# Kernel tuning notes

Hardware: AMD Instinct MI355X
Metric: run time of the kernel (lower is better)

The kernel has to match this reference:

```python
import jax, jax.numpy as jnp
import numpy as np

N_NODES = 100000
N_EDGES = 1600000
IN_CH, HID_CH, OUT_CH = 128, 128, 64
N_GRAPHS = 64


def gcn_conv(x, src, dst, W, b, n_nodes):
    """PyG-style GCNConv: self-loops already included in (src, dst).
    out_i = b + sum_j norm_ij * (x_j @ W), norm_ij = deg_i^-1/2 * deg_j^-1/2."""
    xw = x @ W  # [N, out]
    deg = jax.ops.segment_sum(jnp.ones_like(dst, dtype=xw.dtype), dst,
                              num_segments=n_nodes)  # [N]
    dinv = jnp.where(deg > 0, jax.lax.rsqrt(jnp.maximum(deg, 1e-12)), 0.0)
    norm = dinv[src] * dinv[dst]  # [E]
    msg = xw[src] * norm[:, None]  # gather + scale  [E, out]
    out = jax.ops.segment_sum(msg, dst, num_segments=n_nodes)  # scatter-add
    return out + b


def global_mean_pool(x, batch, n_graphs):
    s = jax.ops.segment_sum(x, batch, num_segments=n_graphs)
    cnt = jax.ops.segment_sum(jnp.ones((x.shape[0],), x.dtype), batch,
                              num_segments=n_graphs)
    return s / jnp.maximum(cnt, 1.0)[:, None]


def setup_inputs() -> dict:
    key = jax.random.key(0)
    ks = jax.random.split(key, 9)
    x = jax.random.normal(ks[0], (N_NODES, IN_CH), dtype=jnp.float32)
    edge_index = jax.random.randint(ks[1], (2, N_EDGES), 0, N_NODES, dtype=jnp.int64)
    batch = jnp.sort(jax.random.randint(ks[2], (N_NODES,), 0, N_GRAPHS, dtype=jnp.int64))
    # Glorot-ish params
    s1 = 1.0 / np.sqrt(IN_CH)
    s2 = 1.0 / np.sqrt(HID_CH)
    W1 = jax.random.normal(ks[3], (IN_CH, HID_CH), jnp.float32) * s1
    b1 = jnp.zeros((HID_CH,), jnp.float32)
    W2 = jax.random.normal(ks[4], (HID_CH, HID_CH), jnp.float32) * s2
    b2 = jnp.zeros((HID_CH,), jnp.float32)
    Wl = jax.random.normal(ks[5], (HID_CH, OUT_CH), jnp.float32) * s2
    bl = jax.random.normal(ks[6], (OUT_CH,), jnp.float32) * 0.01
    return {"x": x, "edge_index": edge_index, "batch": batch,
            "W1": W1, "b1": b1, "W2": W2, "b2": b2, "Wl": Wl, "bl": bl}


def reference(x, edge_index, batch, W1, b1, W2, b2, Wl, bl):
    n = x.shape[0]
    loop = jnp.arange(n, dtype=edge_index.dtype)
    src = jnp.concatenate([edge_index[0], loop])  # add self-loops
    dst = jnp.concatenate([edge_index[1], loop])
    h = jax.nn.relu(gcn_conv(x, src, dst, W1, b1, n))
    h = jax.nn.relu(gcn_conv(h, src, dst, W2, b2, n))
    g = global_mean_pool(h, batch, N_GRAPHS)  # [B, hid]
    return g @ Wl + bl  # [B, out]
```

## Files before the change

kernel.cpp:

```cpp
#include <hip/hip_runtime.h>

#define N_NODESC 100000
#define N_EDGESC 1600000
#define CH 128
#define NG 64
#define OC 64

#define GST_BLKS 391
#define MFMA_BLKS 1563
#define PAD_STRIDE 64
#define SENTINEL N_NODESC

#define BIN_SHIFT 9
#define BIN_W 512
#define NBINS 196
#define BIN_CAP 16384
#define BIN1_BLKS 391
#define E_PER_BIN1 4096

typedef __attribute__((ext_vector_type(8))) short short8;
typedef __attribute__((ext_vector_type(4))) float f32x4;

__device__ __forceinline__ unsigned short f2b_u(float f) {
    union { float f; unsigned int u; } x; x.f = f;
    unsigned int u = x.u;
    return (unsigned short)((u + 0x7fffu + ((u >> 16) & 1u)) >> 16);
}
__device__ __forceinline__ float b2f_lo(unsigned int v) {
    union { unsigned int u; float f; } x; x.u = v << 16; return x.f;
}
__device__ __forceinline__ float b2f_hi(unsigned int v) {
    union { unsigned int u; float f; } x; x.u = v & 0xffff0000u; return x.f;
}

#define WSTR 136
template<int AFP>
__device__ __forceinline__ void mfma_compute(int blk, int t, const void* __restrict__ Ap,
                                             signed char* __restrict__ Oq,
                                             float* __restrict__ osc,
                                             const unsigned short* WsT) {
    int wave = t >> 6, lane = t & 63;
    int quad = lane >> 4, l16 = lane & 15;
    int arow = blk * 64 + wave * 16 + l16;
    bool rowok = arow < N_NODESC;
    f32x4 acc[8] = {};
#pragma unroll
    for (int c = 0; c < 4; ++c) {
        int koff = c * 32 + quad * 8;
        short8 a;
        if (AFP) {
            const float* A = (const float*)Ap;
            float4 f0 = make_float4(0, 0, 0, 0), f1 = make_float4(0, 0, 0, 0);
            if (rowok) {
                f0 = *(const float4*)(A + (size_t)arow * 128 + koff);
                f1 = *(const float4*)(A + (size_t)arow * 128 + koff + 4);
            }
            a[0] = (short)f2b_u(f0.x); a[1] = (short)f2b_u(f0.y);
            a[2] = (short)f2b_u(f0.z); a[3] = (short)f2b_u(f0.w);
            a[4] = (short)f2b_u(f1.x); a[5] = (short)f2b_u(f1.y);
            a[6] = (short)f2b_u(f1.z); a[7] = (short)f2b_u(f1.w);
        } else {
            const unsigned short* A = (const unsigned short*)Ap;
            if (rowok) a = *(const short8*)(A + (size_t)arow * 128 + koff);
            else       a = (short8)(short)0;
        }
#pragma unroll
        for (int tt = 0; tt < 8; ++tt) {
            short8 b = *(const short8*)&WsT[(tt * 16 + l16) * WSTR + koff];
            acc[tt] = __builtin_amdgcn_mfma_f32_16x16x32_bf16(a, b, acc[tt], 0, 0, 0);
        }
    }
    int orow0 = blk * 64 + wave * 16 + quad * 4;
#pragma unroll
    for (int r = 0; r < 4; ++r) {
        int g = orow0 + r;
        float m = 0.f;
#pragma unroll
        for (int tt = 0; tt < 8; ++tt) m = fmaxf(m, fabsf(acc[tt][r]));
        m = fmaxf(m, __shfl_xor(m, 1));
        m = fmaxf(m, __shfl_xor(m, 2));
        m = fmaxf(m, __shfl_xor(m, 4));
        m = fmaxf(m, __shfl_xor(m, 8));
        float inv = m > 0.f ? 127.f / m : 0.f;
        if (g < N_NODESC) {
#pragma unroll
            for (int tt = 0; tt < 8; ++tt)
                Oq[(size_t)g * 128 + tt * 16 + l16] = (signed char)(int)rintf(acc[tt][r] * inv);
            if (l16 == 0) osc[g] = m * (1.f / 127.f);
        }
    }
}

__global__ __launch_bounds__(256) void k_pre(const int* __restrict__ ei,
                                             const int* __restrict__ batch,
                                             const float* __restrict__ W1,
                                             const float* __restrict__ W2,
                                             int* __restrict__ cursor,
                                             unsigned int* __restrict__ binbuf,
                                             unsigned short* __restrict__ Wt1,
                                             unsigned short* __restrict__ Wt2,
                                             int* __restrict__ gstart,
                                             float* __restrict__ xsc) {
    __shared__ int hist[NBINS];
    int b = blockIdx.x, t = threadIdx.x;
    if (b < BIN1_BLKS) {
        for (int i = t; i < NBINS; i += 256) hist[i] = 0;
        __syncthreads();
        int e0 = b * E_PER_BIN1;
#pragma unroll 4
        for (int i = 0; i < E_PER_BIN1 / 256; ++i) {
            int e = e0 + i * 256 + t;
            if (e < N_EDGESC) atomicAdd(&hist[ei[N_EDGESC + e] >> BIN_SHIFT], 1);
        }
        __syncthreads();
        for (int i = t; i < NBINS; i += 256) {
            int c = hist[i];
            hist[i] = c ? atomicAdd(&cursor[i], c) : 0;
        }
        __syncthreads();
#pragma unroll 4
        for (int i = 0; i < E_PER_BIN1 / 256; ++i) {
            int e = e0 + i * 256 + t;
            if (e < N_EDGESC) {
                int d = ei[N_EDGESC + e];
                int s = ei[e];
                int bin = d >> BIN_SHIFT;
                int off = atomicAdd(&hist[bin], 1);
                binbuf[(size_t)bin * BIN_CAP + off] =
                    ((unsigned int)(d & (BIN_W - 1)) << 17) | (unsigned int)s;
            }
        }
    } else if (b < BIN1_BLKS + 64) {
        int i = (b - BIN1_BLKS) * 256 + t;
        int k = i >> 7, c = i & 127;
        Wt1[c * 128 + k] = f2b_u(W1[k * 128 + c]);
    } else if (b < BIN1_BLKS + 128) {
        int i = (b - BIN1_BLKS - 64) * 256 + t;
        int k = i >> 7, c = i & 127;
        Wt2[c * 128 + k] = f2b_u(W2[k * 128 + c]);
    } else {
        int i = (b - BIN1_BLKS - 128) * 256 + t;
        if (i >= N_NODESC) {
            if (i == N_NODESC) xsc[SENTINEL] = 0.f;
            return;
        }
        int bb = batch[i];
        int bp = (i == 0) ? -1 : batch[i - 1];
        for (int g = bp + 1; g <= bb; ++g) gstart[g] = i;
        if (i == N_NODESC - 1)
            for (int g = bb + 1; g <= NG; ++g) gstart[g] = N_NODESC;
    }
}

__global__ __launch_bounds__(256) void k_main(const float* __restrict__ x,
                                              const unsigned short* __restrict__ Wt1,
                                              signed char* __restrict__ xwq,
                                              float* __restrict__ xsc,
                                              const int* __restrict__ cursor,
                                              const unsigned int* __restrict__ binbuf,
                                              int* __restrict__ deg,
                                              float* __restrict__ dinvt,
                                              int* __restrict__ pad) {
    __shared__ unsigned short WsT[128 * WSTR];
    int t = threadIdx.x;
    if (blockIdx.x < NBINS) {
        int bin = blockIdx.x;
        if (bin == 0 && t == 0) dinvt[SENTINEL] = 0.f;
        int* ldeg = (int*)WsT;
        for (int i = t; i < BIN_W; i += 256) ldeg[i] = 0;
        __syncthreads();
        int n = cursor[bin];
        size_t base = (size_t)bin * BIN_CAP;
        for (int i = t; i < n; i += 256) {
            unsigned int rec = binbuf[base + i];
            int dl = rec >> 17;
            int s = rec & 0x1FFFF;
            int slot = atomicAdd(&ldeg[dl], 1) & (PAD_STRIDE - 1);
            pad[(size_t)((bin << BIN_SHIFT) + dl) * PAD_STRIDE + slot] = s;
        }
        __syncthreads();
        for (int i = t; i < BIN_W; i += 256) {
            int node = (bin << BIN_SHIFT) + i;
            if (node < N_NODESC) {
                int dg = ldeg[i];
                if (dg > PAD_STRIDE) dg = PAD_STRIDE;
                deg[node] = dg;
                dinvt[node] = rsqrtf((float)(dg + 1));
                int r8 = (dg + 7) & ~7;
                for (int j = dg; j < r8; ++j)
                    pad[(size_t)node * PAD_STRIDE + j] = SENTINEL;
            }
        }
    } else {
        int blk = blockIdx.x - NBINS;
        const uint4* wsrc = (const uint4*)Wt1;
        for (int idx = t; idx < 2048; idx += 256) {
            int row = idx >> 4, sub = idx & 15;
            *((uint4*)&WsT[row * WSTR] + sub) = wsrc[row * 16 + sub];
        }
        __syncthreads();
        mfma_compute<1>(blk, t, x, xwq, xsc, WsT);
    }
}

__global__ __launch_bounds__(256) void k_mfma2(const unsigned short* __restrict__ A,
                                               const unsigned short* __restrict__ Wt,
                                               signed char* __restrict__ Oq,
                                               float* __restrict__ osc) {
    __shared__ unsigned short WsT[128 * WSTR];
    int t = threadIdx.x;
    {
        const uint4* wsrc = (const uint4*)Wt;
        for (int idx = t; idx < 2048; idx += 256) {
            int row = idx >> 4, sub = idx & 15;
            *((uint4*)&WsT[row * WSTR] + sub) = wsrc[row * 16 + sub];
        }
    }
    __syncthreads();
    mfma_compute<0>(blockIdx.x, t, A, Oq, osc, WsT);
}

#define ACCQ(lo, hi, wk)                                                    \
    acc[0] += wk * (float)((int)((lo) << 24) >> 24);                        \
    acc[1] += wk * (float)((int)((lo) << 16) >> 24);                        \
    acc[2] += wk * (float)((int)((lo) <<  8) >> 24);                        \
    acc[3] += wk * (float)((int)(lo) >> 24);                                \
    acc[4] += wk * (float)((int)((hi) << 24) >> 24);                        \
    acc[5] += wk * (float)((int)((hi) << 16) >> 24);                        \
    acc[6] += wk * (float)((int)((hi) <<  8) >> 24);                        \
    acc[7] += wk * (float)((int)(hi) >> 24);

__device__ __forceinline__ void group_accum(const signed char* __restrict__ xwq,
                                            const float* __restrict__ dinvt,
                                            const float* __restrict__ xsc,
                                            const int* __restrict__ pad,
                                            int base, int l16, int n8,
                                            float* acc) {
    if (n8 <= 0) return;
    const int4* prow = (const int4*)&pad[base];
    int4 p0 = prow[0], p1 = prow[1];
    for (int kb = 0; kb < n8; ++kb) {
        int s[8] = {p0.x, p0.y, p0.z, p0.w, p1.x, p1.y, p1.z, p1.w};
        float w[8];
        uint2 v[8];
#pragma unroll
        for (int k = 0; k < 8; ++k) {
            w[k] = dinvt[s[k]] * xsc[s[k]];
            v[k] = *(const uint2*)&xwq[(size_t)(unsigned int)s[k] * 128 + l16 * 8];
        }
        int nk = (kb + 1 < n8) ? kb + 1 : kb;
        int4 q0 = prow[nk * 2], q1 = prow[nk * 2 + 1];
#pragma unroll
        for (int k = 0; k < 8; ++k) {
            ACCQ(v[k].x, v[k].y, w[k])
        }
        p0 = q0; p1 = q1;
    }
}

__global__ __launch_bounds__(256) void k_gather1(const signed char* __restrict__ xwq,
                                                 const float* __restrict__ xsc,
                                                 const int* __restrict__ deg,
                                                 const float* __restrict__ dinvt,
                                                 const int* __restrict__ pad,
                                                 const float* __restrict__ bias,
                                                 unsigned int* __restrict__ outp) {
    int t = threadIdx.x;
    int lane = t & 63, w = t >> 6;
    int g = lane >> 4, l16 = lane & 15;
    int node = blockIdx.x * 16 + w * 4 + g;
    int dg = deg[node];
    float wn = dinvt[node];
    float wsn = wn * xsc[node];
    uint2 vs = *(const uint2*)&xwq[(size_t)(unsigned int)node * 128 + l16 * 8];
    float acc[8] = {0.f, 0.f, 0.f, 0.f, 0.f, 0.f, 0.f, 0.f};
    ACCQ(vs.x, vs.y, wsn)
    group_accum(xwq, dinvt, xsc, pad, node * PAD_STRIDE, l16, (dg + 7) >> 3, acc);
    float4 bA = *(const float4*)&bias[l16 * 8];
    float4 bB = *(const float4*)&bias[l16 * 8 + 4];
    float o0 = fmaxf(bA.x + wn * acc[0], 0.f);
    float o1 = fmaxf(bA.y + wn * acc[1], 0.f);
    float o2 = fmaxf(bA.z + wn * acc[2], 0.f);
    float o3 = fmaxf(bA.w + wn * acc[3], 0.f);
    float o4 = fmaxf(bB.x + wn * acc[4], 0.f);
    float o5 = fmaxf(bB.y + wn * acc[5], 0.f);
    float o6 = fmaxf(bB.z + wn * acc[6], 0.f);
    float o7 = fmaxf(bB.w + wn * acc[7], 0.f);
    uint4 ov;
    ov.x = ((unsigned int)f2b_u(o1) << 16) | (unsigned int)f2b_u(o0);
    ov.y = ((unsigned int)f2b_u(o3) << 16) | (unsigned int)f2b_u(o2);
    ov.z = ((unsigned int)f2b_u(o5) << 16) | (unsigned int)f2b_u(o4);
    ov.w = ((unsigned int)f2b_u(o7) << 16) | (unsigned int)f2b_u(o6);
    *(uint4*)&outp[(unsigned int)node * 64 + l16 * 4] = ov;
}

__global__ __launch_bounds__(256) void k_gather_pool(const signed char* __restrict__ xwq,
                                                     const float* __restrict__ xsc,
                                                     const int* __restrict__ deg,
                                                     const float* __restrict__ dinvt,
                                                     const int* __restrict__ pad,
                                                     const float* __restrict__ bias,
                                                     const int* __restrict__ batch,
                                                     float* __restrict__ gpart) {
    __shared__ float lds[4 * 128];
    int t = threadIdx.x, w = t >> 6, lane = t & 63;
    int g = lane >> 4, l16 = lane & 15;
    int base = blockIdx.x * 16;
    int node = base + w * 4 + g;
    int dg = deg[node];
    float wn = dinvt[node];
    float wsn = wn * xsc[node];
    uint2 vs = *(const uint2*)&xwq[(size_t)(unsigned int)node * 128 + l16 * 8];
    float acc[8] = {0.f, 0.f, 0.f, 0.f, 0.f, 0.f, 0.f, 0.f};
    ACCQ(vs.x, vs.y, wsn)
    group_accum(xwq, dinvt, xsc, pad, node * PAD_STRIDE, l16, (dg + 7) >> 3, acc);
    float4 bA = *(const float4*)&bias[l16 * 8];
    float4 bB = *(const float4*)&bias[l16 * 8 + 4];
    float o[8];
    o[0] = fmaxf(bA.x + wn * acc[0], 0.f);
    o[1] = fmaxf(bA.y + wn * acc[1], 0.f);
    o[2] = fmaxf(bA.z + wn * acc[2], 0.f);
    o[3] = fmaxf(bA.w + wn * acc[3], 0.f);
    o[4] = fmaxf(bB.x + wn * acc[4], 0.f);
    o[5] = fmaxf(bB.y + wn * acc[5], 0.f);
    o[6] = fmaxf(bB.z + wn * acc[6], 0.f);
    o[7] = fmaxf(bB.w + wn * acc[7], 0.f);
    bool fast = batch[base] == batch[base + 15];
    if (fast) {
#pragma unroll
        for (int j = 0; j < 8; ++j) {
            float v = o[j];
            v += __shfl_xor(v, 16);
            v += __shfl_xor(v, 32);
            o[j] = v;
        }
        if (lane < 16) {
#pragma unroll
            for (int j = 0; j < 8; ++j) lds[w * 128 + l16 * 8 + j] = o[j];
        }
        __syncthreads();
        if (t < 128) {
            float v = lds[t] + lds[128 + t] + lds[256 + t] + lds[384 + t];
            atomicAdd(&gpart[batch[base] * 128 + t], v);
        }
    } else {
        int gb = batch[node];
#pragma unroll
        for (int j = 0; j < 8; ++j)
            atomicAdd(&gpart[gb * 128 + l16 * 8 + j], o[j]);
    }
}

__global__ void k_final(const float* __restrict__ gpart, const int* __restrict__ gstart,
                        const float* __restrict__ Wl, const float* __restrict__ bl,
                        float* __restrict__ out) {
    __shared__ float gs[128];
    int b = blockIdx.x;
    int o = threadIdx.x;
    gs[o] = gpart[b * 128 + o];
    gs[o + 64] = gpart[b * 128 + 64 + o];
    __syncthreads();
    int cnt = gstart[b + 1] - gstart[b];
    float sc = 1.f / (float)(cnt > 0 ? cnt : 1);
    float sum = 0.f;
    for (int k = 0; k < 128; ++k) sum += gs[k] * Wl[k * 64 + o];
    out[b * 64 + o] = bl[o] + sc * sum;
}

extern "C" void kernel_launch(void* const* d_in, const int* in_sizes, int n_in,
                              void* d_out, int out_size, void* d_ws, size_t ws_size,
                              hipStream_t stream) {
    const float* x    = (const float*)d_in[0];
    const int*   ei   = (const int*)d_in[1];
    const int*   batch= (const int*)d_in[2];
    const float* W1   = (const float*)d_in[3];
    const float* b1   = (const float*)d_in[4];
    const float* W2   = (const float*)d_in[5];
    const float* b2   = (const float*)d_in[6];
    const float* Wl   = (const float*)d_in[7];
    const float* bl   = (const float*)d_in[8];
    float* out = (float*)d_out;

    char* ws = (char*)d_ws;
    signed char* xwq = (signed char*)ws; ws += (size_t)(N_NODESC + 1) * CH;
    unsigned short* h_b = (unsigned short*)ws; ws += (size_t)N_NODESC * CH * 2;
    unsigned short* Wt1 = (unsigned short*)ws; ws += (size_t)CH * CH * 2;
    unsigned short* Wt2 = (unsigned short*)ws; ws += (size_t)CH * CH * 2;
    int*   cursor = (int*)ws;   ws += (size_t)NBINS * 4;
    float* gpart  = (float*)ws; ws += (size_t)NG * CH * 4;
    int*   deg    = (int*)ws;   ws += (size_t)N_NODESC * 4;
    float* dinvt  = (float*)ws; ws += (size_t)(N_NODESC + 4) * 4;
    float* xsc    = (float*)ws; ws += (size_t)(N_NODESC + 4) * 4;
    int*   pad    = (int*)ws;   ws += (size_t)N_NODESC * PAD_STRIDE * 4;
    unsigned int* binbuf = (unsigned int*)ws; ws += (size_t)NBINS * BIN_CAP * 4;
    int*   gstart = (int*)ws;   ws += (NG + 8) * 4;

    hipMemsetAsync(cursor, 0, (size_t)NBINS * 4 + (size_t)NG * CH * 4, stream);

    k_pre<<<BIN1_BLKS + 128 + GST_BLKS, 256, 0, stream>>>(ei, batch, W1, W2,
        cursor, binbuf, Wt1, Wt2, gstart, xsc);
    k_main<<<NBINS + MFMA_BLKS, 256, 0, stream>>>(x, Wt1, xwq, xsc, cursor, binbuf,
                                                  deg, dinvt, pad);

    k_gather1<<<N_NODESC / 16, 256, 0, stream>>>(xwq, xsc, deg, dinvt, pad, b1,
                                                 (unsigned int*)h_b);
    k_mfma2<<<MFMA_BLKS, 256, 0, stream>>>(h_b, Wt2, xwq, xsc);
    k_gather_pool<<<N_NODESC / 16, 256, 0, stream>>>(xwq, xsc, deg, dinvt, pad, b2,
                                                     batch, gpart);

    k_final<<<NG, 64, 0, stream>>>(gpart, gstart, Wl, bl, out);
}
```

Before: 293.4 us.

## Process two nodes per lane group and precompute per-node gather weights

Each 16-lane group in the two gather kernels now accumulates two destination nodes with interleaved neighbor batches, and the grid is halved. This is meant to put more independent loads in flight per thread and hide gather latency. A new small kernel precomputes dinv*scale per node before each gather, so every neighbor needs one weight load instead of two. The cost is two extra kernel launches, higher register pressure, and divergence when the two nodes have different degrees.

```diff
diff --git a/kernel.cpp b/kernel.cpp
--- a/kernel.cpp
+++ b/kernel.cpp
@@ -25,12 +25,6 @@
     union { float f; unsigned int u; } x; x.f = f;
     unsigned int u = x.u;
     return (unsigned short)((u + 0x7fffu + ((u >> 16) & 1u)) >> 16);
-}
-__device__ __forceinline__ float b2f_lo(unsigned int v) {
-    union { unsigned int u; float f; } x; x.u = v << 16; return x.f;
-}
-__device__ __forceinline__ float b2f_hi(unsigned int v) {
-    union { unsigned int u; float f; } x; x.u = v & 0xffff0000u; return x.f;
 }
 
 #define WSTR 136
@@ -220,46 +214,43 @@
     mfma_compute<0>(blockIdx.x, t, A, Oq, osc, WsT);
 }
 
-#define ACCQ(lo, hi, wk)                                                    \
-    acc[0] += wk * (float)((int)((lo) << 24) >> 24);                        \
-    acc[1] += wk * (float)((int)((lo) << 16) >> 24);                        \
-    acc[2] += wk * (float)((int)((lo) <<  8) >> 24);                        \
-    acc[3] += wk * (float)((int)(lo) >> 24);                                \
-    acc[4] += wk * (float)((int)((hi) << 24) >> 24);                        \
-    acc[5] += wk * (float)((int)((hi) << 16) >> 24);                        \
-    acc[6] += wk * (float)((int)((hi) <<  8) >> 24);                        \
-    acc[7] += wk * (float)((int)(hi) >> 24);
-
-__device__ __forceinline__ void group_accum(const signed char* __restrict__ xwq,
-                                            const float* __restrict__ dinvt,
-                                            const float* __restrict__ xsc,
-                                            const int* __restrict__ pad,
-                                            int base, int l16, int n8,
-                                            float* acc) {
-    if (n8 <= 0) return;
-    const int4* prow = (const int4*)&pad[base];
-    int4 p0 = prow[0], p1 = prow[1];
-    for (int kb = 0; kb < n8; ++kb) {
-        int s[8] = {p0.x, p0.y, p0.z, p0.w, p1.x, p1.y, p1.z, p1.w};
-        float w[8];
-        uint2 v[8];
-#pragma unroll
-        for (int k = 0; k < 8; ++k) {
-            w[k] = dinvt[s[k]] * xsc[s[k]];
-            v[k] = *(const uint2*)&xwq[(size_t)(unsigned int)s[k] * 128 + l16 * 8];
-        }
-        int nk = (kb + 1 < n8) ? kb + 1 : kb;
-        int4 q0 = prow[nk * 2], q1 = prow[nk * 2 + 1];
-#pragma unroll
-        for (int k = 0; k < 8; ++k) {
-            ACCQ(v[k].x, v[k].y, w[k])
-        }
-        p0 = q0; p1 = q1;
-    }
+__global__ __launch_bounds__(256) void k_wsc(const float* __restrict__ dinvt,
+                                             const float* __restrict__ xsc,
+                                             float* __restrict__ wsc) {
+    int i = blockIdx.x * 256 + threadIdx.x;
+    if (i <= N_NODESC) wsc[i] = dinvt[i] * xsc[i];
+}
+
+__device__ __forceinline__ void accq(float* acc, unsigned int lo, unsigned int hi, float wk) {
+    acc[0] += wk * (float)((int)(lo << 24) >> 24);
+    acc[1] += wk * (float)((int)(lo << 16) >> 24);
+    acc[2] += wk * (float)((int)(lo <<  8) >> 24);
+    acc[3] += wk * (float)((int)lo >> 24);
+    acc[4] += wk * (float)((int)(hi << 24) >> 24);
+    acc[5] += wk * (float)((int)(hi << 16) >> 24);
+    acc[6] += wk * (float)((int)(hi <<  8) >> 24);
+    acc[7] += wk * (float)((int)hi >> 24);
+}
+
+__device__ __forceinline__ void accum8(const signed char* __restrict__ xwq,
+                                       const float* __restrict__ wsc,
+                                       const int4* __restrict__ prow,
+                                       int kb, int l16, float* acc) {
+    int4 p0 = prow[kb * 2], p1 = prow[kb * 2 + 1];
+    int s[8] = {p0.x, p0.y, p0.z, p0.w, p1.x, p1.y, p1.z, p1.w};
+    float w[8];
+    uint2 v[8];
+#pragma unroll
+    for (int k = 0; k < 8; ++k) {
+        w[k] = wsc[s[k]];
+        v[k] = *(const uint2*)&xwq[(size_t)(unsigned int)s[k] * 128 + l16 * 8];
+    }
+#pragma unroll
+    for (int k = 0; k < 8; ++k) accq(acc, v[k].x, v[k].y, w[k]);
 }
 
 __global__ __launch_bounds__(256) void k_gather1(const signed char* __restrict__ xwq,
-                                                 const float* __restrict__ xsc,
+                                                 const float* __restrict__ wsc,
                                                  const int* __restrict__ deg,
                                                  const float* __restrict__ dinvt,
                                                  const int* __restrict__ pad,
@@ -268,34 +259,51 @@
     int t = threadIdx.x;
     int lane = t & 63, w = t >> 6;
     int g = lane >> 4, l16 = lane & 15;
-    int node = blockIdx.x * 16 + w * 4 + g;
-    int dg = deg[node];
-    float wn = dinvt[node];
-    float wsn = wn * xsc[node];
-    uint2 vs = *(const uint2*)&xwq[(size_t)(unsigned int)node * 128 + l16 * 8];
-    float acc[8] = {0.f, 0.f, 0.f, 0.f, 0.f, 0.f, 0.f, 0.f};
-    ACCQ(vs.x, vs.y, wsn)
-    group_accum(xwq, dinvt, xsc, pad, node * PAD_STRIDE, l16, (dg + 7) >> 3, acc);
+    int nA = blockIdx.x * 32 + w * 8 + g * 2;
+    int nB = nA + 1;
+    int dgA = deg[nA], dgB = deg[nB];
+    float wnA = dinvt[nA], wnB = dinvt[nB];
+    float wsA = wsc[nA], wsB = wsc[nB];
+    uint2 vsA = *(const uint2*)&xwq[(size_t)(unsigned int)nA * 128 + l16 * 8];
+    uint2 vsB = *(const uint2*)&xwq[(size_t)(unsigned int)nB * 128 + l16 * 8];
+    float accA[8] = {0.f, 0.f, 0.f, 0.f, 0.f, 0.f, 0.f, 0.f};
+    float accB[8] = {0.f, 0.f, 0.f, 0.f, 0.f, 0.f, 0.f, 0.f};
+    accq(accA, vsA.x, vsA.y, wsA);
+    accq(accB, vsB.x, vsB.y, wsB);
+    int nbA = (dgA + 7) >> 3, nbB = (dgB + 7) >> 3;
+    int nmax = nbA > nbB ? nbA : nbB;
+    const int4* prA = (const int4*)&pad[nA * PAD_STRIDE];
+    const int4* prB = (const int4*)&pad[nB * PAD_STRIDE];
+    for (int kb = 0; kb < nmax; ++kb) {
+        if (kb < nbA) accum8(xwq, wsc, prA, kb, l16, accA);
+        if (kb < nbB) accum8(xwq, wsc, prB, kb, l16, accB);
+    }
     float4 bA = *(const float4*)&bias[l16 * 8];
     float4 bB = *(const float4*)&bias[l16 * 8 + 4];
-    float o0 = fmaxf(bA.x + wn * acc[0], 0.f);
-    float o1 = fmaxf(bA.y + wn * acc[1], 0.f);
-    float o2 = fmaxf(bA.z + wn * acc[2], 0.f);
-    float o3 = fmaxf(bA.w + wn * acc[3], 0.f);
-    float o4 = fmaxf(bB.x + wn * acc[4], 0.f);
-    float o5 = fmaxf(bB.y + wn * acc[5], 0.f);
-    float o6 = fmaxf(bB.z + wn * acc[6], 0.f);
-    float o7 = fmaxf(bB.w + wn * acc[7], 0.f);
-    uint4 ov;
-    ov.x = ((unsigned int)f2b_u(o1) << 16) | (unsigned int)f2b_u(o0);
-    ov.y = ((unsigned int)f2b_u(o3) << 16) | (unsigned int)f2b_u(o2);
-    ov.z = ((unsigned int)f2b_u(o5) << 16) | (unsigned int)f2b_u(o4);
-    ov.w = ((unsigned int)f2b_u(o7) << 16) | (unsigned int)f2b_u(o6);
-    *(uint4*)&outp[(unsigned int)node * 64 + l16 * 4] = ov;
+    float oA[8], oB[8];
+    oA[0] = fmaxf(bA.x + wnA * accA[0], 0.f); oA[1] = fmaxf(bA.y + wnA * accA[1], 0.f);
+    oA[2] = fmaxf(bA.z + wnA * accA[2], 0.f); oA[3] = fmaxf(bA.w + wnA * accA[3], 0.f);
+    oA[4] = fmaxf(bB.x + wnA * accA[4], 0.f); oA[5] = fmaxf(bB.y + wnA * accA[5], 0.f);
+    oA[6] = fmaxf(bB.z + wnA * accA[6], 0.f); oA[7] = fmaxf(bB.w + wnA * accA[7], 0.f);
+    oB[0] = fmaxf(bA.x + wnB * accB[0], 0.f); oB[1] = fmaxf(bA.y + wnB * accB[1], 0.f);
+    oB[2] = fmaxf(bA.z + wnB * accB[2], 0.f); oB[3] = fmaxf(bA.w + wnB * accB[3], 0.f);
+    oB[4] = fmaxf(bB.x + wnB * accB[4], 0.f); oB[5] = fmaxf(bB.y + wnB * accB[5], 0.f);
+    oB[6] = fmaxf(bB.z + wnB * accB[6], 0.f); oB[7] = fmaxf(bB.w + wnB * accB[7], 0.f);
+    uint4 ovA, ovB;
+    ovA.x = ((unsigned int)f2b_u(oA[1]) << 16) | (unsigned int)f2b_u(oA[0]);
+    ovA.y = ((unsigned int)f2b_u(oA[3]) << 16) | (unsigned int)f2b_u(oA[2]);
+    ovA.z = ((unsigned int)f2b_u(oA[5]) << 16) | (unsigned int)f2b_u(oA[4]);
+    ovA.w = ((unsigned int)f2b_u(oA[7]) << 16) | (unsigned int)f2b_u(oA[6]);
+    ovB.x = ((unsigned int)f2b_u(oB[1]) << 16) | (unsigned int)f2b_u(oB[0]);
+    ovB.y = ((unsigned int)f2b_u(oB[3]) << 16) | (unsigned int)f2b_u(oB[2]);
+    ovB.z = ((unsigned int)f2b_u(oB[5]) << 16) | (unsigned int)f2b_u(oB[4]);
+    ovB.w = ((unsigned int)f2b_u(oB[7]) << 16) | (unsigned int)f2b_u(oB[6]);
+    *(uint4*)&outp[(unsigned int)nA * 64 + l16 * 4] = ovA;
+    *(uint4*)&outp[(unsigned int)nB * 64 + l16 * 4] = ovB;
 }
 
 __global__ __launch_bounds__(256) void k_gather_pool(const signed char* __restrict__ xwq,
-                                                     const float* __restrict__ xsc,
+                                                     const float* __restrict__ wsc,
                                                      const int* __restrict__ deg,
                                                      const float* __restrict__ dinvt,
                                                      const int* __restrict__ pad,
@@ -305,38 +313,49 @@
     __shared__ float lds[4 * 128];
     int t = threadIdx.x, w = t >> 6, lane = t & 63;
     int g = lane >> 4, l16 = lane & 15;
-    int base = blockIdx.x * 16;
-    int node = base + w * 4 + g;
-    int dg = deg[node];
-    float wn = dinvt[node];
-    float wsn = wn * xsc[node];
-    uint2 vs = *(const uint2*)&xwq[(size_t)(unsigned int)node * 128 + l16 * 8];
-    float acc[8] = {0.f, 0.f, 0.f, 0.f, 0.f, 0.f, 0.f, 0.f};
-    ACCQ(vs.x, vs.y, wsn)
-    group_accum(xwq, dinvt, xsc, pad, node * PAD_STRIDE, l16, (dg + 7) >> 3, acc);
+    int base = blockIdx.x * 32;
+    int nA = base + w * 8 + g * 2;
+    int nB = nA + 1;
+    int dgA = deg[nA], dgB = deg[nB];
+    float wnA = dinvt[nA], wnB = dinvt[nB];
+    float wsA = wsc[nA], wsB = wsc[nB];
+    uint2 vsA = *(const uint2*)&xwq[(size_t)(unsigned int)nA * 128 + l16 * 8];
+    uint2 vsB = *(const uint2*)&xwq[(size_t)(unsigned int)nB * 128 + l16 * 8];
+    float accA[8] = {0.f, 0.f, 0.f, 0.f, 0.f, 0.f, 0.f, 0.f};
+    float accB[8] = {0.f, 0.f, 0.f, 0.f, 0.f, 0.f, 0.f, 0.f};
+    accq(accA, vsA.x, vsA.y, wsA);
+    accq(accB, vsB.x, vsB.y, wsB);
+    int nbA = (dgA + 7) >> 3, nbB = (dgB + 7) >> 3;
+    int nmax = nbA > nbB ? nbA : nbB;
+    const int4* prA = (const int4*)&pad[nA * PAD_STRIDE];
+    const int4* prB = (const int4*)&pad[nB * PAD_STRIDE];
+    for (int kb = 0; kb < nmax; ++kb) {
+        if (kb < nbA) accum8(xwq, wsc, prA, kb, l16, accA);
+        if (kb < nbB) accum8(xwq, wsc, prB, kb, l16, accB);
+    }
     float4 bA = *(const float4*)&bias[l16 * 8];
     float4 bB = *(const float4*)&bias[l16 * 8 + 4];
-    float o[8];
-    o[0] = fmaxf(bA.x + wn * acc[0], 0.f);
-    o[1] = fmaxf(bA.y + wn * acc[1], 0.f);
-    o[2] = fmaxf(bA.z + wn * acc[2], 0.f);
-    o[3] = fmaxf(bA.w + wn * acc[3], 0.f);
-    o[4] = fmaxf(bB.x + wn * acc[4], 0.f);
-    o[5] = fmaxf(bB.y + wn * acc[5], 0.f);
-    o[6] = fmaxf(bB.z + wn * acc[6], 0.f);
-    o[7] = fmaxf(bB.w + wn * acc[7], 0.f);
-    bool fast = batch[base] == batch[base + 15];
+    float oA[8], oB[8];
+    oA[0] = fmaxf(bA.x + wnA * accA[0], 0.f); oA[1] = fmaxf(bA.y + wnA * accA[1], 0.f);
+    oA[2] = fmaxf(bA.z + wnA * accA[2], 0.f); oA[3] = fmaxf(bA.w + wnA * accA[3], 0.f);
+    oA[4] = fmaxf(bB.x + wnA * accA[4], 0.f); oA[5] = fmaxf(bB.y + wnA * accA[5], 0.f);
+    oA[6] = fmaxf(bB.z + wnA * accA[6], 0.f); oA[7] = fmaxf(bB.w + wnA * accA[7], 0.f);
+    oB[0] = fmaxf(bA.x + wnB * accB[0], 0.f); oB[1] = fmaxf(bA.y + wnB * accB[1], 0.f);
+    oB[2] = fmaxf(bA.z + wnB * accB[2], 0.f); oB[3] = fmaxf(bA.w + wnB * accB[3], 0.f);
+    oB[4] = fmaxf(bB.x + wnB * accB[4], 0.f); oB[5] = fmaxf(bB.y + wnB * accB[5], 0.f);
+    oB[6] = fmaxf(bB.z + wnB * accB[6], 0.f); oB[7] = fmaxf(bB.w + wnB * accB[7], 0.f);
+    bool fast = batch[base] == batch[base + 31];
     if (fast) {
 #pragma unroll
         for (int j = 0; j < 8; ++j) {
-            float v = o[j];
+            float v = oA[j] + oB[j];
             v += __shfl_xor(v, 16);
             v += __shfl_xor(v, 32);
-            o[j] = v;
+            oA[j] = v;
         }
         if (lane < 16) {
 #pragma unroll
-            for (int j = 0; j < 8; ++j) lds[w * 128 + l16 * 8 + j] = o[j];
+            for (int j = 0; j < 8; ++j) lds[w * 128 + l16 * 8 + j] = oA[j];
         }
         __syncthreads();
         if (t < 128) {
@@ -344,10 +363,12 @@
             atomicAdd(&gpart[batch[base] * 128 + t], v);
         }
     } else {
-        int gb = batch[node];
-#pragma unroll
-        for (int j = 0; j < 8; ++j)
-            atomicAdd(&gpart[gb * 128 + l16 * 8 + j], o[j]);
+        int gA = batch[nA], gB = batch[nB];
+#pragma unroll
+        for (int j = 0; j < 8; ++j) {
+            atomicAdd(&gpart[gA * 128 + l16 * 8 + j], oA[j]);
+            atomicAdd(&gpart[gB * 128 + l16 * 8 + j], oB[j]);
+        }
     }
 }
 
@@ -391,6 +412,7 @@
     int*   deg    = (int*)ws;   ws += (size_t)N_NODESC * 4;
     float* dinvt  = (float*)ws; ws += (size_t)(N_NODESC + 4) * 4;
     float* xsc    = (float*)ws; ws += (size_t)(N_NODESC + 4) * 4;
+    float* wsc    = (float*)ws; ws += (size_t)(N_NODESC + 4) * 4;
     int*   pad    = (int*)ws;   ws += (size_t)N_NODESC * PAD_STRIDE * 4;
     unsigned int* binbuf = (unsigned int*)ws; ws += (size_t)NBINS * BIN_CAP * 4;
     int*   gstart = (int*)ws;   ws += (NG + 8) * 4;
@@ -401,11 +423,13 @@
         cursor, binbuf, Wt1, Wt2, gstart, xsc);
     k_main<<<NBINS + MFMA_BLKS, 256, 0, stream>>>(x, Wt1, xwq, xsc, cursor, binbuf,
                                                   deg, dinvt, pad);
-
-    k_gather1<<<N_NODESC / 16, 256, 0, stream>>>(xwq, xsc, deg, dinvt, pad, b1,
+    k_wsc<<<GST_BLKS, 256, 0, stream>>>(dinvt, xsc, wsc);
+
+    k_gather1<<<N_NODESC / 32, 256, 0, stream>>>(xwq, wsc, deg, dinvt, pad, b1,
                                                  (unsigned int*)h_b);
     k_mfma2<<<MFMA_BLKS, 256, 0, stream>>>(h_b, Wt2, xwq, xsc);
-    k_gather_pool<<<N_NODESC / 16, 256, 0, stream>>>(xwq, xsc, deg, dinvt, pad, b2,
+    k_wsc<<<GST_BLKS, 256, 0, stream>>>(dinvt, xsc, wsc);
+    k_gather_pool<<<N_NODESC / 32, 256, 0, stream>>>(xwq, wsc, deg, dinvt, pad, b2,
                                                      batch, gpart);
 
     k_final<<<NG, 64, 0, stream>>>(gpart, gstart, Wl, bl, out);
```

After: 285.7 us. 1.03x faster.
